# Kernel tuning notes

Hardware: AMD Instinct MI355X
Metric: run time of the kernel (lower is better)

The kernel has to match this reference:

```python
import jax, jax.numpy as jnp
import numpy as np

N_NODES = 200000
IN_SIZE = 128
OUT_SIZE = 128
N_EDGES = 600000


def setup_inputs() -> dict:
    key = jax.random.key(0)
    k1, k2, k3, k4 = jax.random.split(key, 4)
    embedding = jax.random.normal(k1, (N_NODES, IN_SIZE), dtype=jnp.float32)
    up2down_edge_index = jax.random.randint(k2, (2, N_EDGES), 0, N_NODES, dtype=jnp.int64)
    # GCNConv params (glorot weight, zero bias as in PyG defaults)
    scale = np.sqrt(6.0 / (IN_SIZE + OUT_SIZE)).astype(np.float32)
    W = jax.random.uniform(k3, (IN_SIZE, OUT_SIZE), dtype=jnp.float32, minval=-scale, maxval=scale)
    b = jnp.zeros((OUT_SIZE,), dtype=jnp.float32)
    return {"embedding": embedding, "up2down_edge_index": up2down_edge_index, "W": W, "b": b}


def reference(embedding, up2down_edge_index, W, b):
    # PyG GCNConv: add self-loops, symmetric normalization, linear transform,
    # scatter-sum aggregation, add bias.
    N = embedding.shape[0]
    loops = jnp.arange(N, dtype=up2down_edge_index.dtype)
    src = jnp.concatenate([up2down_edge_index[0], loops])  # message sources
    dst = jnp.concatenate([up2down_edge_index[1], loops])  # message targets

    # degree of each target node (edge_weight = 1)
    deg = jax.ops.segment_sum(jnp.ones_like(src, dtype=embedding.dtype), dst, num_segments=N)
    deg_inv_sqrt = jnp.where(deg > 0, jax.lax.rsqrt(jnp.maximum(deg, 1.0)), 0.0)
    norm = deg_inv_sqrt[src] * deg_inv_sqrt[dst]  # [E+N]

    h = embedding @ W  # [N, out]
    msg = h[src] * norm[:, None]  # gather + scale, [E+N, out]
    out = jax.ops.segment_sum(msg, dst, num_segments=N)  # scatter-add
    return out + b
```

## Files before the change

kernel.cpp:

```cpp
#include <hip/hip_runtime.h>
#include <hip/hip_bf16.h>
#include <stdint.h>

typedef __attribute__((ext_vector_type(8))) short short8v;
typedef __attribute__((ext_vector_type(4))) float f32x4;

__device__ __forceinline__ unsigned short f2bf(float f) {
  unsigned int u = __float_as_uint(f);
  u += 0x7fffu + ((u >> 16) & 1u);
  return (unsigned short)(u >> 16);
}
__device__ __forceinline__ unsigned int pack2bf(float a, float b) {
  return (unsigned int)f2bf(a) | ((unsigned int)f2bf(b) << 16);
}
__device__ __forceinline__ float bf_lo(unsigned int v) { return __uint_as_float(v << 16); }
__device__ __forceinline__ float bf_hi(unsigned int v) { return __uint_as_float(v & 0xffff0000u); }

__global__ void k_prep(uint4* __restrict__ zp, int n16,
                       const float* __restrict__ W, unsigned short* __restrict__ Wfrag) {
  int b = blockIdx.x;
  if (b < 64) {
    int t = b * 256 + threadIdx.x;
    int j = t & 7;
    int lane = (t >> 3) & 63;
    int ktct = t >> 9;
    int kt = ktct & 3, ct = ktct >> 2;
    int col = ct * 16 + (lane & 15);
    int k = kt * 32 + 4 * (lane >> 4) + (j & 3) + 16 * (j >> 2);
    Wfrag[t] = f2bf(W[k * 128 + col]);
  } else {
    int i = (b - 64) * 256 + threadIdx.x;
    if (i < n16) {
      uint4 z; z.x = z.y = z.z = z.w = 0u;
      zp[i] = z;
    }
  }
}

__global__ void k_count(const int* __restrict__ dst, int* deg, int E) {
  int e = blockIdx.x * blockDim.x + threadIdx.x;
  if (e < E) atomicAdd(&deg[dst[e]], 1);
}

__global__ void k_blocksum(const int* __restrict__ deg, int* partials, float* dis, int N) {
  __shared__ int s[256];
  int t = threadIdx.x;
  int i = blockIdx.x * 256 + t;
  int c = (i < N) ? deg[i] : 0;
  if (i < N) dis[i] = rsqrtf((float)(c + 1));
  s[t] = c;
  __syncthreads();
  for (int off = 128; off > 0; off >>= 1) {
    if (t < off) s[t] += s[t + off];
    __syncthreads();
  }
  if (t == 0) partials[blockIdx.x] = s[0];
}

__global__ void k_scan_final2(const int* __restrict__ deg, const int* __restrict__ partials,
                              int* csr_off, int N, int E) {
  __shared__ int s[256];
  __shared__ int base;
  int t = threadIdx.x;
  int accp = 0;
  for (int j = t; j < blockIdx.x; j += 256) accp += partials[j];
  s[t] = accp;
  __syncthreads();
  for (int off = 128; off > 0; off >>= 1) {
    if (t < off) s[t] += s[t + off];
    __syncthreads();
  }
  if (t == 0) base = s[0];
  __syncthreads();
  int i = blockIdx.x * 256 + t;
  int c = (i < N) ? deg[i] : 0;
  s[t] = c;
  __syncthreads();
  for (int off = 1; off < 256; off <<= 1) {
    int v = (t >= off) ? s[t - off] : 0;
    __syncthreads();
    s[t] += v;
    __syncthreads();
  }
  if (i < N) csr_off[i] = base + s[t] - c;
  if (i == 0) csr_off[N] = E;
}

__global__ void k_fill(const int* __restrict__ src, const int* __restrict__ dst,
                       const int* __restrict__ csr_off, int* cursor, int* csr_src, int E) {
  int e = blockIdx.x * blockDim.x + threadIdx.x;
  if (e < E) {
    int d = dst[e];
    int p = atomicAdd(&cursor[d], 1);
    csr_src[csr_off[d] + p] = src[e];
  }
}

__device__ __forceinline__ short8v pack8(float4 a, float4 b) {
  short8v r;
  r[0] = (short)f2bf(a.x); r[1] = (short)f2bf(a.y);
  r[2] = (short)f2bf(a.z); r[3] = (short)f2bf(a.w);
  r[4] = (short)f2bf(b.x); r[5] = (short)f2bf(b.y);
  r[6] = (short)f2bf(b.z); r[7] = (short)f2bf(b.w);
  return r;
}


#define GLOAD(XB, DD, TT, HAS)                                                  \
  do {                                                                          \
    if (HAS) {                                                                  \
      int row_ = (TT) * 16 + lr;                                                \
      if (row_ < N) {                                                           \
        const float* xp_ = X + (size_t)row_ * 128 + 4 * lg;                     \
        _Pragma("unroll") for (int q = 0; q < 4; ++q) {                         \
          XB[2 * q]     = *(const float4*)(xp_ + q * 32);                       \
          XB[2 * q + 1] = *(const float4*)(xp_ + q * 32 + 16);                  \
        }                                                                       \
        DD = dis[row_];                                                         \
      } else {                                                                  \
        _Pragma("unroll") for (int q = 0; q < 8; ++q) {                         \
          XB[q].x = XB[q].y = XB[q].z = XB[q].w = 0.f;                          \
        }                                                                       \
        DD = 0.f;                                                               \
      }                                                                         \
    }                                                                           \
  } while (0)

#define GCOMPUTE(XB, DD, TT)                                                    \
  do {                                                                          \
    short8v afr[4];                                                             \
    _Pragma("unroll") for (int kt = 0; kt < 4; ++kt)                            \
        afr[kt] = pack8(XB[2 * kt], XB[2 * kt + 1]);                            \
    int row_ = (TT) * 16 + lr;                                                  \
    bool wr_ = row_ < N;                                                        \
    unsigned short* hp_ = hs + (size_t)row_ * 128;                              \
    float dd_ = DD;                                                             \
    _Pragma("unroll") for (int cp = 0; cp < 4; ++cp) {                          \
      f32x4 a0 = {0.f, 0.f, 0.f, 0.f}, a1 = {0.f, 0.f, 0.f, 0.f};               \
      _Pragma("unroll") for (int kt = 0; kt < 4; ++kt)                          \
          a0 = __builtin_amdgcn_mfma_f32_16x16x32_bf16(wreg[(2 * cp) * 4 + kt], \
                                                       afr[kt], a0, 0, 0, 0);   \
      _Pragma("unroll") for (int kt = 0; kt < 4; ++kt)                          \
          a1 = __builtin_amdgcn_mfma_f32_16x16x32_bf16(                         \
              wreg[(2 * cp + 1) * 4 + kt], afr[kt], a1, 0, 0, 0);               \
      unsigned int u0x = pack2bf(a0[0] * dd_, a0[1] * dd_);                     \
      unsigned int u0y = pack2bf(a0[2] * dd_, a0[3] * dd_);                     \
      unsigned int u1x = pack2bf(a1[0] * dd_, a1[1] * dd_);                     \
      unsigned int u1y = pack2bf(a1[2] * dd_, a1[3] * dd_);                     \
      int s_ = lg & 1;                                                          \
      unsigned int sx = s_ ? u0x : u1x, sy = s_ ? u0y : u1y;                    \
      unsigned int rx = (unsigned int)__shfl_xor((int)sx, 16);                  \
      unsigned int ry = (unsigned int)__shfl_xor((int)sy, 16);                  \
      uint4 uu;                                                                 \
      if (s_ == 0) { uu.x = u0x; uu.y = u0y; uu.z = rx; uu.w = ry; }            \
      else         { uu.x = rx; uu.y = ry; uu.z = u1x; uu.w = u1y; }            \
      int cb = (s_ ? (2 * cp + 1) : (2 * cp)) * 16 + 8 * (lg >> 1);             \
      if (wr_) *(uint4*)(hp_ + cb) = uu;                                        \
    }                                                                           \
  } while (0)

__global__ __launch_bounds__(256, 2) void k_gemm5(const float* __restrict__ X,
     const unsigned short* __restrict__ Wfrag, const float* __restrict__ dis,
     unsigned short* __restrict__ hs, int N, int ntile) {
  int lane = threadIdx.x & 63;
  int gw = (blockIdx.x * blockDim.x + threadIdx.x) >> 6;
  int nw = (gridDim.x * blockDim.x) >> 6;
  int lr = lane & 15, lg = lane >> 4;

  short8v wreg[32];
  #pragma unroll
  for (int f = 0; f < 32; ++f)
    wreg[f] = *(const short8v*)(Wfrag + (size_t)(f * 64 + lane) * 8);

  int tile = gw;
  if (tile >= ntile) return;

  float4 xv[8], nx[8];
  float d0 = 0.f, d1 = 0.f;
  GLOAD(xv, d0, tile, true);

  for (;;) {
    int t1 = tile + nw;
    bool h1 = t1 < ntile;
    GLOAD(nx, d1, t1, h1);
    GCOMPUTE(xv, d0, tile);
    if (!h1) break;
    int t2 = t1 + nw;
    bool h2 = t2 < ntile;
    GLOAD(xv, d0, t2, h2);
    GCOMPUTE(nx, d1, t1);
    if (!h2) break;
    tile = t2;
  }
}

__device__ __forceinline__ void acc8(float* a, uint4 g) {
  a[0] += bf_lo(g.x); a[1] += bf_hi(g.x);
  a[2] += bf_lo(g.y); a[3] += bf_hi(g.y);
  a[4] += bf_lo(g.z); a[5] += bf_hi(g.z);
  a[6] += bf_lo(g.w); a[7] += bf_hi(g.w);
}

__global__ __launch_bounds__(256) void k_agg2(const unsigned short* __restrict__ hs_,
     const int* __restrict__ csr_src, const int* __restrict__ csr_off,
     const float* __restrict__ dis, const float* __restrict__ bias,
     float* __restrict__ out, int N) {
  const uint4* hs = (const uint4*)hs_;
  int lane = threadIdx.x & 63;
  int c = lane & 15;
  int base = lane & 48;
  int gid = (blockIdx.x * blockDim.x + threadIdx.x) >> 4;
  int G = (gridDim.x * blockDim.x) >> 4;
  int i0 = (int)(((long long)gid * N) / G);
  int i1 = (int)(((long long)(gid + 1) * N) / G);
  if (i0 >= i1) return;
  float4 bA = ((const float4*)bias)[c * 2];
  float4 bB = ((const float4*)bias)[c * 2 + 1];
  int e1prev = csr_off[i0];
  for (int i = i0; i < i1; ++i) {
    int e0 = e1prev;
    int e1 = csr_off[i + 1];
    e1prev = e1;
    float a[8];
    uint4 sv = hs[(size_t)i * 16 + c];
    a[0] = bf_lo(sv.x); a[1] = bf_hi(sv.x);
    a[2] = bf_lo(sv.y); a[3] = bf_hi(sv.y);
    a[4] = bf_lo(sv.z); a[5] = bf_hi(sv.z);
    a[6] = bf_lo(sv.w); a[7] = bf_hi(sv.w);
    int e = e0;
    while (e < e1) {
      int p = e + c;
      int myidx = (p < e1) ? csr_src[p] : 0;
      int kb = (e1 - e < 16) ? (e1 - e) : 16;
      int k = 0;
      for (; k + 8 <= kb; k += 8) {
        int s[8];
        #pragma unroll
        for (int q = 0; q < 8; ++q) s[q] = __shfl(myidx, base + k + q);
        uint4 g[8];
        #pragma unroll
        for (int q = 0; q < 8; ++q) g[q] = hs[(size_t)s[q] * 16 + c];
        #pragma unroll
        for (int q = 0; q < 8; ++q) acc8(a, g[q]);
      }
      for (; k < kb; k += 4) {
        int s0 = __shfl(myidx, base + k);
        int s1 = __shfl(myidx, base + k + 1);
        int s2 = __shfl(myidx, base + k + 2);
        int s3 = __shfl(myidx, base + k + 3);
        bool v1 = (k + 1 < kb), v2 = (k + 2 < kb), v3 = (k + 3 < kb);
        uint4 g0 = hs[(size_t)s0 * 16 + c];
        uint4 g1 = hs[(size_t)(v1 ? s1 : i) * 16 + c];
        uint4 g2 = hs[(size_t)(v2 ? s2 : i) * 16 + c];
        uint4 g3 = hs[(size_t)(v3 ? s3 : i) * 16 + c];
        if (!v1) { g1.x = g1.y = g1.z = g1.w = 0u; }
        if (!v2) { g2.x = g2.y = g2.z = g2.w = 0u; }
        if (!v3) { g3.x = g3.y = g3.z = g3.w = 0u; }
        acc8(a, g0); acc8(a, g1); acc8(a, g2); acc8(a, g3);
      }
      e += kb;
    }
    float di = dis[i];
    float4 o0, o1;
    o0.x = fmaf(di, a[0], bA.x); o0.y = fmaf(di, a[1], bA.y);
    o0.z = fmaf(di, a[2], bA.z); o0.w = fmaf(di, a[3], bA.w);
    o1.x = fmaf(di, a[4], bB.x); o1.y = fmaf(di, a[5], bB.y);
    o1.z = fmaf(di, a[6], bB.z); o1.w = fmaf(di, a[7], bB.w);
    float4* op = (float4*)(out + (size_t)i * 128);
    op[c * 2] = o0;
    op[c * 2 + 1] = o1;
  }
}

extern "C" void kernel_launch(void* const* d_in, const int* in_sizes, int n_in,
                              void* d_out, int out_size, void* d_ws, size_t ws_size,
                              hipStream_t stream) {
  const float* X    = (const float*)d_in[0];
  const int*   edge = (const int*)d_in[1];
  const float* W    = (const float*)d_in[2];
  const float* bias = (const float*)d_in[3];
  float* out = (float*)d_out;
  int N = in_sizes[0] / 128;
  int E = in_sizes[1] / 2;
  const int* srcArr = edge;
  const int* dstArr = edge + E;

  char* w = (char*)d_ws;
  auto align = [](size_t x) { return (x + 255) & ~(size_t)255; };
  size_t o = 0;
  int*   deg      = (int*)(w + o);   o += align((size_t)N * 4);
  int*   cursor   = (int*)(w + o);   o += align((size_t)N * 4);
  float* dis      = (float*)(w + o); o += align((size_t)N * 4);
  int*   csr_off  = (int*)(w + o);   o += align(((size_t)N + 1) * 4);
  int*   csr_src  = (int*)(w + o);   o += align((size_t)E * 4);
  int*   partials = (int*)(w + o);   o += align((size_t)4096 * 4);
  unsigned short* Wfrag = (unsigned short*)(w + o); o += align((size_t)16384 * 2);
  unsigned short* hs    = (unsigned short*)(w + o);

  int nbN = (N + 255) / 256;
  int nbE = (E + 255) / 256;
  int ntile = (N + 15) / 16;

  size_t zbytes = align((size_t)N * 4) + align((size_t)N * 4);
  int n16 = (int)(zbytes / 16);
  k_prep<<<64 + (n16 + 255) / 256, 256, 0, stream>>>((uint4*)deg, n16, W, Wfrag);
  k_count<<<nbE, 256, 0, stream>>>(dstArr, deg, E);
  k_blocksum<<<nbN, 256, 0, stream>>>(deg, partials, dis, N);
  k_scan_final2<<<nbN, 256, 0, stream>>>(deg, partials, csr_off, N, E);
  k_fill<<<nbE, 256, 0, stream>>>(srcArr, dstArr, csr_off, cursor, csr_src, E);
  k_gemm5<<<512, 256, 0, stream>>>(X, Wfrag, dis, hs, N, ntile);
  k_agg2<<<2048, 256, 0, stream>>>(hs, csr_src, csr_off, dis, bias, out, N);
}
```

Measured before the change: 151.5 us.

## Stream CSR indices per node range with prefetch in aggregation kernel

The aggregation kernel now treats each 16-lane group's node range as one continuous edge stream. It loads 16 source indices per window and prefetches the next window, and it also prefetches the next node's self-loop row, instead of reloading indices for every node. With about 4 edges per node this should cut index loads and partial-window overhead, and the remainder path handles 1-3 edges with fewer wasted gathers. The GEMM kernel's float4 vectors are swapped for native ext_vector f32x4, which mainly affects code generation. The wrap-around logic in the remainder path adds more complexity at window boundaries.

```diff
diff --git a/kernel.cpp b/kernel.cpp
--- a/kernel.cpp
+++ b/kernel.cpp
@@ -96,12 +96,12 @@
   }
 }
 
-__device__ __forceinline__ short8v pack8(float4 a, float4 b) {
+__device__ __forceinline__ short8v pack8(f32x4 a, f32x4 b) {
   short8v r;
-  r[0] = (short)f2bf(a.x); r[1] = (short)f2bf(a.y);
-  r[2] = (short)f2bf(a.z); r[3] = (short)f2bf(a.w);
-  r[4] = (short)f2bf(b.x); r[5] = (short)f2bf(b.y);
-  r[6] = (short)f2bf(b.z); r[7] = (short)f2bf(b.w);
+  r[0] = (short)f2bf(a[0]); r[1] = (short)f2bf(a[1]);
+  r[2] = (short)f2bf(a[2]); r[3] = (short)f2bf(a[3]);
+  r[4] = (short)f2bf(b[0]); r[5] = (short)f2bf(b[1]);
+  r[6] = (short)f2bf(b[2]); r[7] = (short)f2bf(b[3]);
   return r;
 }
 
@@ -113,13 +113,13 @@
       if (row_ < N) {                                                           \
         const float* xp_ = X + (size_t)row_ * 128 + 4 * lg;                     \
         _Pragma("unroll") for (int q = 0; q < 4; ++q) {                         \
-          XB[2 * q]     = *(const float4*)(xp_ + q * 32);                       \
-          XB[2 * q + 1] = *(const float4*)(xp_ + q * 32 + 16);                  \
+          XB[2 * q]     = *(const f32x4*)(xp_ + q * 32);                        \
+          XB[2 * q + 1] = *(const f32x4*)(xp_ + q * 32 + 16);                   \
         }                                                                       \
         DD = dis[row_];                                                         \
       } else {                                                                  \
         _Pragma("unroll") for (int q = 0; q < 8; ++q) {                         \
-          XB[q].x = XB[q].y = XB[q].z = XB[q].w = 0.f;                          \
+          XB[q][0] = XB[q][1] = XB[q][2] = XB[q][3] = 0.f;                      \
         }                                                                       \
         DD = 0.f;                                                               \
       }                                                                         \
@@ -175,7 +175,7 @@
   int tile = gw;
   if (tile >= ntile) return;
 
-  float4 xv[8], nx[8];
+  f32x4 xv[8], nx[8];
   float d0 = 0.f, d1 = 0.f;
   GLOAD(xv, d0, tile, true);
 
@@ -201,7 +201,7 @@
   a[6] += bf_lo(g.w); a[7] += bf_hi(g.w);
 }
 
-__global__ __launch_bounds__(256) void k_agg2(const unsigned short* __restrict__ hs_,
+__global__ __launch_bounds__(256) void k_agg3(const unsigned short* __restrict__ hs_,
      const int* __restrict__ csr_src, const int* __restrict__ csr_off,
      const float* __restrict__ dis, const float* __restrict__ bias,
      float* __restrict__ out, int N) {
@@ -216,50 +216,65 @@
   if (i0 >= i1) return;
   float4 bA = ((const float4*)bias)[c * 2];
   float4 bB = ((const float4*)bias)[c * 2 + 1];
-  int e1prev = csr_off[i0];
+
+  int E0 = csr_off[i0];
+  int E1 = csr_off[i1];
+  int curidx  = (E0 + c < E1) ? csr_src[E0 + c] : 0;
+  int nbase   = E0 + 16;
+  int nextidx = (nbase + c < E1) ? csr_src[nbase + c] : 0;
+  int wpos = 0;
+  int e1prev = E0;
+  uint4 sv = hs[(size_t)i0 * 16 + c];
+
   for (int i = i0; i < i1; ++i) {
-    int e0 = e1prev;
     int e1 = csr_off[i + 1];
+    int cnt = e1 - e1prev;
     e1prev = e1;
     float a[8];
-    uint4 sv = hs[(size_t)i * 16 + c];
     a[0] = bf_lo(sv.x); a[1] = bf_hi(sv.x);
     a[2] = bf_lo(sv.y); a[3] = bf_hi(sv.y);
     a[4] = bf_lo(sv.z); a[5] = bf_hi(sv.z);
     a[6] = bf_lo(sv.w); a[7] = bf_hi(sv.w);
-    int e = e0;
-    while (e < e1) {
-      int p = e + c;
-      int myidx = (p < e1) ? csr_src[p] : 0;
-      int kb = (e1 - e < 16) ? (e1 - e) : 16;
+    if (i + 1 < i1) sv = hs[(size_t)(i + 1) * 16 + c];
+
+    while (cnt > 0) {
+      int avail = 16 - wpos;
+      int take = (cnt < avail) ? cnt : avail;
       int k = 0;
-      for (; k + 8 <= kb; k += 8) {
-        int s[8];
-        #pragma unroll
-        for (int q = 0; q < 8; ++q) s[q] = __shfl(myidx, base + k + q);
-        uint4 g[8];
-        #pragma unroll
-        for (int q = 0; q < 8; ++q) g[q] = hs[(size_t)s[q] * 16 + c];
-        #pragma unroll
-        for (int q = 0; q < 8; ++q) acc8(a, g[q]);
+      for (; k + 4 <= take; k += 4) {
+        int s0 = __shfl(curidx, base + wpos + k);
+        int s1 = __shfl(curidx, base + wpos + k + 1);
+        int s2 = __shfl(curidx, base + wpos + k + 2);
+        int s3 = __shfl(curidx, base + wpos + k + 3);
+        uint4 g0 = hs[(size_t)s0 * 16 + c];
+        uint4 g1 = hs[(size_t)s1 * 16 + c];
+        uint4 g2 = hs[(size_t)s2 * 16 + c];
+        uint4 g3 = hs[(size_t)s3 * 16 + c];
+        acc8(a, g0); acc8(a, g1); acc8(a, g2); acc8(a, g3);
       }
-      for (; k < kb; k += 4) {
-        int s0 = __shfl(myidx, base + k);
-        int s1 = __shfl(myidx, base + k + 1);
-        int s2 = __shfl(myidx, base + k + 2);
-        int s3 = __shfl(myidx, base + k + 3);
-        bool v1 = (k + 1 < kb), v2 = (k + 2 < kb), v3 = (k + 3 < kb);
+      if (k < take) {
+        int r = take - k;
+        int s0 = __shfl(curidx, base + wpos + k);
+        int s1 = __shfl(curidx, base + ((wpos + k + 1) & 15));
+        int s2 = __shfl(curidx, base + ((wpos + k + 2) & 15));
+        bool v1 = (r > 1), v2 = (r > 2);
         uint4 g0 = hs[(size_t)s0 * 16 + c];
         uint4 g1 = hs[(size_t)(v1 ? s1 : i) * 16 + c];
         uint4 g2 = hs[(size_t)(v2 ? s2 : i) * 16 + c];
-        uint4 g3 = hs[(size_t)(v3 ? s3 : i) * 16 + c];
         if (!v1) { g1.x = g1.y = g1.z = g1.w = 0u; }
         if (!v2) { g2.x = g2.y = g2.z = g2.w = 0u; }
-        if (!v3) { g3.x = g3.y = g3.z = g3.w = 0u; }
-        acc8(a, g0); acc8(a, g1); acc8(a, g2); acc8(a, g3);
+        acc8(a, g0); acc8(a, g1); acc8(a, g2);
+        k = take;
       }
-      e += kb;
+      wpos += take; cnt -= take;
+      if (wpos == 16) {
+        curidx = nextidx;
+        wpos = 0;
+        nbase += 16;
+        nextidx = (nbase + c < E1) ? csr_src[nbase + c] : 0;
+      }
     }
+
     float di = dis[i];
     float4 o0, o1;
     o0.x = fmaf(di, a[0], bA.x); o0.y = fmaf(di, a[1], bA.y);
@@ -309,5 +324,5 @@
   k_scan_final2<<<nbN, 256, 0, stream>>>(deg, partials, csr_off, N, E);
   k_fill<<<nbE, 256, 0, stream>>>(srcArr, dstArr, csr_off, cursor, csr_src, E);
   k_gemm5<<<512, 256, 0, stream>>>(X, Wfrag, dis, hs, N, ntile);
-  k_agg2<<<2048, 256, 0, stream>>>(hs, csr_src, csr_off, dis, bias, out, N);
-}
+  k_agg3<<<2048, 256, 0, stream>>>(hs, csr_src, csr_off, dis, bias, out, N);
+}
```

Measured after the change: 160.4 us. 1.06x slower.

## Replace two-pass prefix scan with single-pass decoupled look-back scan

Applied to the files above, without the earlier changes.

Merges the block-sum and final-scan kernels into one single-pass scan. Each block takes a dynamic block id from an atomic counter and publishes its aggregate and inclusive prefix through flagged 64-bit status words that later blocks read back. This removes one kernel launch and the quadratic re-summing of partials in the old final scan. In exchange it adds spin-waiting on predecessor status words and extends the zeroed workspace to cover the status array and counter. The GEMM tile buffers also switch from float4 to native vector types, which is cosmetic.

```diff
diff --git a/kernel.cpp b/kernel.cpp
--- a/kernel.cpp
+++ b/kernel.cpp
@@ -42,38 +42,19 @@
   if (e < E) atomicAdd(&deg[dst[e]], 1);
 }
 
-__global__ void k_blocksum(const int* __restrict__ deg, int* partials, float* dis, int N) {
+__global__ void k_scan1(const int* __restrict__ deg, float* __restrict__ dis,
+                        int* __restrict__ csr_off, unsigned long long* __restrict__ stat,
+                        int* __restrict__ counter, int N, int E) {
+  __shared__ int sbid;
   __shared__ int s[256];
+  __shared__ int sprev;
   int t = threadIdx.x;
-  int i = blockIdx.x * 256 + t;
+  if (t == 0) sbid = atomicAdd(counter, 1);
+  __syncthreads();
+  int bid = sbid;
+  int i = bid * 256 + t;
   int c = (i < N) ? deg[i] : 0;
   if (i < N) dis[i] = rsqrtf((float)(c + 1));
-  s[t] = c;
-  __syncthreads();
-  for (int off = 128; off > 0; off >>= 1) {
-    if (t < off) s[t] += s[t + off];
-    __syncthreads();
-  }
-  if (t == 0) partials[blockIdx.x] = s[0];
-}
-
-__global__ void k_scan_final2(const int* __restrict__ deg, const int* __restrict__ partials,
-                              int* csr_off, int N, int E) {
-  __shared__ int s[256];
-  __shared__ int base;
-  int t = threadIdx.x;
-  int accp = 0;
-  for (int j = t; j < blockIdx.x; j += 256) accp += partials[j];
-  s[t] = accp;
-  __syncthreads();
-  for (int off = 128; off > 0; off >>= 1) {
-    if (t < off) s[t] += s[t + off];
-    __syncthreads();
-  }
-  if (t == 0) base = s[0];
-  __syncthreads();
-  int i = blockIdx.x * 256 + t;
-  int c = (i < N) ? deg[i] : 0;
   s[t] = c;
   __syncthreads();
   for (int off = 1; off < 256; off <<= 1) {
@@ -82,7 +63,30 @@
     s[t] += v;
     __syncthreads();
   }
-  if (i < N) csr_off[i] = base + s[t] - c;
+  int total = s[255];
+  if (t == 0) {
+    unsigned long long fl = (bid == 0) ? 2ull : 1ull;
+    __hip_atomic_store(&stat[bid], (fl << 62) | (unsigned int)total,
+                       __ATOMIC_RELEASE, __HIP_MEMORY_SCOPE_AGENT);
+    int prev = 0;
+    if (bid > 0) {
+      int p = bid - 1;
+      for (;;) {
+        unsigned long long v = __hip_atomic_load(&stat[p], __ATOMIC_ACQUIRE,
+                                                 __HIP_MEMORY_SCOPE_AGENT);
+        unsigned long long fl2 = v >> 62;
+        if (fl2 == 0) continue;
+        prev += (int)(v & 0xffffffffull);
+        if (fl2 == 2ull) break;
+        --p;
+      }
+      __hip_atomic_store(&stat[bid], (2ull << 62) | (unsigned int)(prev + total),
+                         __ATOMIC_RELEASE, __HIP_MEMORY_SCOPE_AGENT);
+    }
+    sprev = prev;
+  }
+  __syncthreads();
+  if (i < N) csr_off[i] = sprev + s[t] - c;
   if (i == 0) csr_off[N] = E;
 }
 
@@ -96,12 +100,12 @@
   }
 }
 
-__device__ __forceinline__ short8v pack8(float4 a, float4 b) {
+__device__ __forceinline__ short8v pack8(f32x4 a, f32x4 b) {
   short8v r;
-  r[0] = (short)f2bf(a.x); r[1] = (short)f2bf(a.y);
-  r[2] = (short)f2bf(a.z); r[3] = (short)f2bf(a.w);
-  r[4] = (short)f2bf(b.x); r[5] = (short)f2bf(b.y);
-  r[6] = (short)f2bf(b.z); r[7] = (short)f2bf(b.w);
+  r[0] = (short)f2bf(a[0]); r[1] = (short)f2bf(a[1]);
+  r[2] = (short)f2bf(a[2]); r[3] = (short)f2bf(a[3]);
+  r[4] = (short)f2bf(b[0]); r[5] = (short)f2bf(b[1]);
+  r[6] = (short)f2bf(b[2]); r[7] = (short)f2bf(b[3]);
   return r;
 }
 
@@ -113,13 +117,13 @@
       if (row_ < N) {                                                           \
         const float* xp_ = X + (size_t)row_ * 128 + 4 * lg;                     \
         _Pragma("unroll") for (int q = 0; q < 4; ++q) {                         \
-          XB[2 * q]     = *(const float4*)(xp_ + q * 32);                       \
-          XB[2 * q + 1] = *(const float4*)(xp_ + q * 32 + 16);                  \
+          XB[2 * q]     = *(const f32x4*)(xp_ + q * 32);                        \
+          XB[2 * q + 1] = *(const f32x4*)(xp_ + q * 32 + 16);                   \
         }                                                                       \
         DD = dis[row_];                                                         \
       } else {                                                                  \
         _Pragma("unroll") for (int q = 0; q < 8; ++q) {                         \
-          XB[q].x = XB[q].y = XB[q].z = XB[q].w = 0.f;                          \
+          XB[q][0] = XB[q][1] = XB[q][2] = XB[q][3] = 0.f;                      \
         }                                                                       \
         DD = 0.f;                                                               \
       }                                                                         \
@@ -175,7 +179,7 @@
   int tile = gw;
   if (tile >= ntile) return;
 
-  float4 xv[8], nx[8];
+  f32x4 xv[8], nx[8];
   float d0 = 0.f, d1 = 0.f;
   GLOAD(xv, d0, tile, true);
 
@@ -285,28 +289,28 @@
   const int* srcArr = edge;
   const int* dstArr = edge + E;
 
+  int nbN = (N + 255) / 256;
+  int nbE = (E + 255) / 256;
+  int ntile = (N + 15) / 16;
+
   char* w = (char*)d_ws;
   auto align = [](size_t x) { return (x + 255) & ~(size_t)255; };
   size_t o = 0;
   int*   deg      = (int*)(w + o);   o += align((size_t)N * 4);
   int*   cursor   = (int*)(w + o);   o += align((size_t)N * 4);
+  unsigned long long* stat = (unsigned long long*)(w + o); o += align((size_t)nbN * 8);
+  int*   counter  = (int*)(w + o);   o += align((size_t)256);
+  size_t zend = o;
   float* dis      = (float*)(w + o); o += align((size_t)N * 4);
   int*   csr_off  = (int*)(w + o);   o += align(((size_t)N + 1) * 4);
   int*   csr_src  = (int*)(w + o);   o += align((size_t)E * 4);
-  int*   partials = (int*)(w + o);   o += align((size_t)4096 * 4);
   unsigned short* Wfrag = (unsigned short*)(w + o); o += align((size_t)16384 * 2);
   unsigned short* hs    = (unsigned short*)(w + o);
 
-  int nbN = (N + 255) / 256;
-  int nbE = (E + 255) / 256;
-  int ntile = (N + 15) / 16;
-
-  size_t zbytes = align((size_t)N * 4) + align((size_t)N * 4);
-  int n16 = (int)(zbytes / 16);
-  k_prep<<<64 + (n16 + 255) / 256, 256, 0, stream>>>((uint4*)deg, n16, W, Wfrag);
+  int n16 = (int)(zend / 16);
+  k_prep<<<64 + (n16 + 255) / 256, 256, 0, stream>>>((uint4*)d_ws, n16, W, Wfrag);
   k_count<<<nbE, 256, 0, stream>>>(dstArr, deg, E);
-  k_blocksum<<<nbN, 256, 0, stream>>>(deg, partials, dis, N);
-  k_scan_final2<<<nbN, 256, 0, stream>>>(deg, partials, csr_off, N, E);
+  k_scan1<<<nbN, 256, 0, stream>>>(deg, dis, csr_off, stat, counter, N, E);
   k_fill<<<nbE, 256, 0, stream>>>(srcArr, dstArr, csr_off, cursor, csr_src, E);
   k_gemm5<<<512, 256, 0, stream>>>(X, Wfrag, dis, hs, N, ntile);
   k_agg2<<<2048, 256, 0, stream>>>(hs, csr_src, csr_off, dis, bias, out, N);
```

After: 361.6 us. +138.7%, slower.
